# Kernel optimization log

Hardware: AMD Instinct MI355X
Metric: run time of the kernel (lower is better)

The kernel has to match this reference:

```python
import jax, jax.numpy as jnp
import numpy as np

B, C, H, W = 2, 256, 32, 32
PK, CK = 256, 256


def setup_inputs() -> dict:
    key = jax.random.key(0)
    ks = jax.random.split(key, 9)
    s = 1.0 / np.sqrt(C)
    return {
        'x': jax.random.normal(ks[0], (B, C, H, W), jnp.float32),
        'primary_indices': jax.random.randint(ks[1], (B, PK), 0, B * H * W),
        'compare_indices': jax.random.randint(ks[2], (B, CK), 0, B * H * W),
        'pre_w': jax.random.uniform(ks[3], (3, C, C), jnp.float32, -s, s),
        'pre_b': jax.random.uniform(ks[4], (3, C), jnp.float32, -s, s),
        'post_w': jax.random.uniform(ks[5], (2, C, C), jnp.float32, -s, s),
        'post_b': jax.random.uniform(ks[6], (2, C), jnp.float32, -s, s),
        'post_out_w': jax.random.uniform(ks[7], (2, C), jnp.float32, -s, s),
        'post_out_b': jax.random.uniform(ks[8], (2,), jnp.float32, -s, s),
    }


def reference(x, primary_indices, compare_indices, pre_w, pre_b,
              post_w, post_b, post_out_w, post_out_b):
    # pre_compare: stack of 1x1 convs (c->c->c->c), ReLU between layers
    h = x
    for i in range(3):
        h = jnp.einsum('bchw,oc->bohw', h, pre_w[i]) + pre_b[i][None, :, None, None]
        if i < 2:
            h = jax.nn.relu(h)
    bs, c, hh, ww = h.shape
    # flatten to [bs*h*w, c] node features (matches torch transpose+reshape)
    flat = h.reshape(bs, c, hh * ww).transpose(0, 2, 1).reshape(bs * hh * ww, c)
    # gather primary / compare node features with global flat indices
    xp = flat[primary_indices.reshape(-1)].reshape(bs, -1, c).transpose(0, 2, 1)  # [b,c,pk]
    xc = flat[compare_indices.reshape(-1)].reshape(bs, -1, c).transpose(0, 2, 1)  # [b,c,ck]
    # broadcast pairwise squared difference -> [b,c,pk,ck]
    xx = (xp[:, :, :, None] - xc[:, :, None, :]) ** 2
    # post_compare: 1x1 conv stack c->c->c->2, ReLU between layers
    g = xx
    for i in range(2):
        g = jax.nn.relu(jnp.einsum('bcpq,oc->bopq', g, post_w[i]) + post_b[i][None, :, None, None])
    out = jnp.einsum('bcpq,oc->bopq', g, post_out_w) + post_out_b[None, :, None, None]
    return out  # [b, 2, pk, ck]
```

## Files before the change

### kernel.cpp

```cpp
#include <hip/hip_runtime.h>

typedef unsigned short u16;
typedef short bf16x8 __attribute__((ext_vector_type(8)));
typedef float f32x4 __attribute__((ext_vector_type(4)));
typedef u16 u16x4 __attribute__((ext_vector_type(4)));

__device__ __forceinline__ float b2f(u16 h) {
  unsigned u = ((unsigned)h) << 16;
  return __builtin_bit_cast(float, u);
}
__device__ __forceinline__ u16 f2b(float f) {
  unsigned u = __builtin_bit_cast(unsigned, f);
  u = u + 0x7fffu + ((u >> 16) & 1u);
  return (u16)(u >> 16);
}
__device__ __forceinline__ void gld_lds16(const void* g, void* l) {
  __builtin_amdgcn_global_load_lds(
      (__attribute__((address_space(1))) void*)(g),
      (__attribute__((address_space(3))) void*)(l), 16, 0, 0);
}

__global__ void dense_edge_prep(const float* __restrict__ x,
                                const float* __restrict__ pre_w,
                                const float* __restrict__ post_w,
                                u16* __restrict__ wb, u16* __restrict__ xt) {
  const int blk = blockIdx.x;
  const int t = threadIdx.x;
  if (blk < 160) {
    const int id = blk * 256 + t;
    const int layer = id >> 13;
    const int sid = id & 8191;
    const int m = sid >> 5;
    const int s8 = sid & 31;
    const float* src = (layer < 2) ? (post_w + layer * 65536)
                                   : (pre_w + (layer - 2) * 65536);
    u16* dst = wb + layer * 65536;
    f32x4 a = *(const f32x4*)(src + m * 256 + s8 * 8);
    f32x4 c = *(const f32x4*)(src + m * 256 + s8 * 8 + 4);
    bf16x8 o;
#pragma unroll
    for (int j = 0; j < 4; j++) o[j] = (short)f2b(a[j]);
#pragma unroll
    for (int j = 0; j < 4; j++) o[4 + j] = (short)f2b(c[j]);
    *(bf16x8*)(dst + (s8 * 256 + m) * 8) = o;
  } else {
    __shared__ float tile[32 * 65];
    const int xb = blk - 160;
    const int b = xb >> 7;
    const int ct = (xb >> 4) & 7;
    const int ht = xb & 15;
    const int c0 = ct * 32, hw0 = ht * 64;
#pragma unroll
    for (int rep = 0; rep < 8; rep++) {
      const int idx = rep * 256 + t;
      const int cl = idx >> 6, hl = idx & 63;
      tile[cl * 65 + hl] = x[(b * 256 + c0 + cl) * 1024 + hw0 + hl];
    }
    __syncthreads();
    const int hl = t >> 2, c8 = t & 3;
    bf16x8 o;
#pragma unroll
    for (int i = 0; i < 8; i++) o[i] = (short)f2b(tile[(c8 * 8 + i) * 65 + hl]);
    *(bf16x8*)(xt + (b * 1024 + hw0 + hl) * 256 + c0 + c8 * 8) = o;
  }
}

__global__ __launch_bounds__(256, 2) void dense_edge_pre(
    const u16* __restrict__ xt, const u16* __restrict__ wpre,
    const float* __restrict__ preb, u16* __restrict__ flat) {
  __shared__ u16 feat[2][4096];
  const int t = threadIdx.x;
  const int wv = t >> 6, ln = t & 63;
  const int nb = blockIdx.x * 16;
  const int q4 = ln >> 4, r15 = ln & 15;

#pragma unroll
  for (int i = 0; i < 2; i++) {
    const int slot = wv * 128 + i * 64 + ln;
    const int s8 = slot >> 4, nl = slot & 15;
    gld_lds16(xt + (nb + nl) * 256 + s8 * 8, &feat[0][slot * 8]);
  }
  __syncthreads();

#pragma unroll
  for (int l = 0; l < 3; l++) {
    const u16* wl = wpre + l * 65536;
    f32x4 acc[4];
    f32x4 zero = {0.f, 0.f, 0.f, 0.f};
#pragma unroll
    for (int mt = 0; mt < 4; mt++) acc[mt] = zero;
#pragma unroll
    for (int s = 0; s < 8; s++) {
      bf16x8 bv = *(const bf16x8*)(&feat[l & 1][((s * 4 + q4) * 16 + r15) * 8]);
#pragma unroll
      for (int mt = 0; mt < 4; mt++) {
        bf16x8 av = *(const bf16x8*)(wl + ((s * 4 + q4) * 256 + wv * 64 + mt * 16 + r15) * 8);
        acc[mt] = __builtin_amdgcn_mfma_f32_16x16x32_bf16(av, bv, acc[mt], 0, 0, 0);
      }
    }
    if (l < 2) {
#pragma unroll
      for (int mt = 0; mt < 4; mt++) {
        const int o = wv * 64 + mt * 16 + q4 * 4;
        f32x4 bb = *(const f32x4*)(preb + l * 256 + o);
        u16x4 pk;
#pragma unroll
        for (int r = 0; r < 4; r++) {
          float v = fmaxf(acc[mt][r] + bb[r], 0.f);
          pk[r] = f2b(v);
        }
        *(u16x4*)(&feat[(l + 1) & 1][((o >> 3) * 16 + r15) * 8 + (o & 7)]) = pk;
      }
      __syncthreads();
    } else {
#pragma unroll
      for (int mt = 0; mt < 4; mt++) {
        const int o = wv * 64 + mt * 16 + q4 * 4;
        f32x4 bb = *(const f32x4*)(preb + 512 + o);
        u16x4 pk;
#pragma unroll
        for (int r = 0; r < 4; r++) pk[r] = f2b(acc[mt][r] + bb[r]);
        *(u16x4*)(flat + (nb + r15) * 256 + o) = pk;
      }
    }
  }
}

__global__ __launch_bounds__(512, 2) void dense_edge_main(
    const u16* __restrict__ flat, const int* __restrict__ pidx,
    const int* __restrict__ cidx, const u16* __restrict__ w1s,
    const u16* __restrict__ w2s, const float* __restrict__ b1,
    const float* __restrict__ b2, const float* __restrict__ w3,
    const float* __restrict__ b3, float* __restrict__ out) {
  __shared__ u16 xxbuf[16384];
  __shared__ u16 t1buf[16384];
  __shared__ float pbuf[4][2][64];

  const int t = threadIdx.x;
  const int wv = t >> 6;
  const int ln = t & 63;
  const int q4 = ln >> 4, r15 = ln & 15;
  const bool prod = wv < 4;
  const int cw = wv & 3;
  const int blk = blockIdx.x;
  const int tile0 = blk * 8;
  const int b = tile0 >> 10;
  const int pt = (tile0 >> 5) & 31;
  const int qt0 = tile0 & 31;
  const int p0 = pt * 8;

  const u16* wsrc = prod ? w1s : w2s;
  bf16x8 af_w[4][8];
#pragma unroll
  for (int s = 0; s < 8; s++)
#pragma unroll
    for (int mt = 0; mt < 4; mt++)
      af_w[mt][s] = *(const bf16x8*)(wsrc + ((s * 4 + q4) * 256 + cw * 64 + mt * 16 + r15) * 8);

  int pn = 0;
  if (prod) pn = pidx[b * 256 + p0 + (ln >> 3)];
  const u16* prow = flat + pn * 256 + cw * 64;

#pragma unroll 1
  for (int j = 0; j <= 8; j++) {
    if (prod) {
      if (j < 8) {
        const int qn = cidx[b * 256 + (qt0 + j) * 8 + (ln & 7)];
        const u16* qrow = flat + qn * 256 + cw * 64;
#pragma unroll
        for (int i = 0; i < 8; i++) {
          bf16x8 av = *(const bf16x8*)(prow + i * 8);
          bf16x8 bv = *(const bf16x8*)(qrow + i * 8);
          bf16x8 ov;
#pragma unroll
          for (int jj = 0; jj < 8; jj++) {
            float d = b2f((u16)av[jj]) - b2f((u16)bv[jj]);
            ov[jj] = (short)f2b(d * d);
          }
          *(bf16x8*)(xxbuf + ((cw * 8 + i) * 64 + ln) * 8) = ov;
        }
      }
    } else if (j > 0) {
      f32x4 acc[4][4];
      {
        f32x4 zero = {0.f, 0.f, 0.f, 0.f};
#pragma unroll
        for (int mt = 0; mt < 4; mt++)
#pragma unroll
          for (int nt = 0; nt < 4; nt++) acc[mt][nt] = zero;
      }
#pragma unroll
      for (int s = 0; s < 8; s++) {
        bf16x8 bfr[4];
#pragma unroll
        for (int nt = 0; nt < 4; nt++)
          bfr[nt] = *(const bf16x8*)(t1buf + ((s * 4 + q4) * 64 + nt * 16 + r15) * 8);
#pragma unroll
        for (int mt = 0; mt < 4; mt++)
#pragma unroll
          for (int nt = 0; nt < 4; nt++)
            acc[mt][nt] = __builtin_amdgcn_mfma_f32_16x16x32_bf16(af_w[mt][s], bfr[nt], acc[mt][nt], 0, 0, 0);
      }
      float part[2][4] = {{0.f, 0.f, 0.f, 0.f}, {0.f, 0.f, 0.f, 0.f}};
#pragma unroll
      for (int mt = 0; mt < 4; mt++) {
        const int o = cw * 64 + mt * 16 + q4 * 4;
        f32x4 bb = *(const f32x4*)(b2 + o);
        f32x4 w3a = *(const f32x4*)(w3 + o);
        f32x4 w3b = *(const f32x4*)(w3 + 256 + o);
#pragma unroll
        for (int nt = 0; nt < 4; nt++) {
#pragma unroll
          for (int r = 0; r < 4; r++) {
            float v = fmaxf(acc[mt][nt][r] + bb[r], 0.f);
            part[0][nt] += v * w3a[r];
            part[1][nt] += v * w3b[r];
          }
        }
      }
#pragma unroll
      for (int o3 = 0; o3 < 2; o3++)
#pragma unroll
        for (int nt = 0; nt < 4; nt++) {
          part[o3][nt] += __shfl_xor(part[o3][nt], 16, 64);
          part[o3][nt] += __shfl_xor(part[o3][nt], 32, 64);
        }
      if (q4 == 0) {
#pragma unroll
        for (int o3 = 0; o3 < 2; o3++)
#pragma unroll
          for (int nt = 0; nt < 4; nt++)
            pbuf[cw][o3][nt * 16 + r15] = part[o3][nt];
      }
    }
    __syncthreads();

    if (prod) {
      if (j < 8) {
        f32x4 acc[4][4];
        {
          f32x4 zero = {0.f, 0.f, 0.f, 0.f};
#pragma unroll
          for (int mt = 0; mt < 4; mt++)
#pragma unroll
            for (int nt = 0; nt < 4; nt++) acc[mt][nt] = zero;
        }
#pragma unroll
        for (int s = 0; s < 8; s++) {
          bf16x8 bfr[4];
#pragma unroll
          for (int nt = 0; nt < 4; nt++)
            bfr[nt] = *(const bf16x8*)(xxbuf + ((s * 4 + q4) * 64 + nt * 16 + r15) * 8);
#pragma unroll
          for (int mt = 0; mt < 4; mt++)
#pragma unroll
            for (int nt = 0; nt < 4; nt++)
              acc[mt][nt] = __builtin_amdgcn_mfma_f32_16x16x32_bf16(af_w[mt][s], bfr[nt], acc[mt][nt], 0, 0, 0);
        }
#pragma unroll
        for (int mt = 0; mt < 4; mt++) {
          const int o = cw * 64 + mt * 16 + q4 * 4;
          f32x4 bb = *(const f32x4*)(b1 + o);
#pragma unroll
          for (int nt = 0; nt < 4; nt++) {
            const int nn = nt * 16 + r15;
            u16x4 pk;
#pragma unroll
            for (int r = 0; r < 4; r++) {
              float v = fmaxf(acc[mt][nt][r] + bb[r], 0.f);
              pk[r] = f2b(v);
            }
            *(u16x4*)(t1buf + ((o >> 3) * 64 + nn) * 8 + (o & 7)) = pk;
          }
        }
      }
    } else if (j > 0) {
      const int idx = t & 255;
      if (idx < 128) {
        const int o3 = idx >> 6;
        const int n = idx & 63;
        float v = pbuf[0][o3][n] + pbuf[1][o3][n] + pbuf[2][o3][n] + pbuf[3][o3][n] + b3[o3];
        out[((b * 2 + o3) * 256 + p0 + (n >> 3)) * 256 + (qt0 + j - 1) * 8 + (n & 7)] = v;
      }
    }
    __syncthreads();
  }
}

extern "C" void kernel_launch(void* const* d_in, const int* in_sizes, int n_in,
                              void* d_out, int out_size, void* d_ws, size_t ws_size,
                              hipStream_t stream) {
  (void)in_sizes; (void)n_in; (void)out_size; (void)ws_size;
  const float* x          = (const float*)d_in[0];
  const int*   pidx       = (const int*)d_in[1];
  const int*   cidx       = (const int*)d_in[2];
  const float* pre_w      = (const float*)d_in[3];
  const float* pre_b      = (const float*)d_in[4];
  const float* post_w     = (const float*)d_in[5];
  const float* post_b     = (const float*)d_in[6];
  const float* post_out_w = (const float*)d_in[7];
  const float* post_out_b = (const float*)d_in[8];
  float* out = (float*)d_out;

  u16* ws   = (u16*)d_ws;
  u16* wb   = ws;
  u16* w1s  = wb;
  u16* w2s  = wb + 65536;
  u16* wpre = wb + 131072;
  u16* xt   = ws + 327680;
  u16* flat = ws + 851968;

  dense_edge_prep<<<416, 256, 0, stream>>>(x, pre_w, post_w, wb, xt);
  dense_edge_pre<<<128, 256, 0, stream>>>(xt, wpre, pre_b, flat);
  dense_edge_main<<<256, 512, 0, stream>>>(flat, pidx, cidx, w1s, w2s,
                                           post_b, post_b + 256,
                                           post_out_w, post_out_b, out);
}
```

Before: 124.3 us.

## Pipeline main kernel with double-buffered t1 and async compare-row prefetch

Restructures the main loop so each iteration has a single phase between barriers. Producer waves run GEMM1 into a double-buffered t1buf while consumer waves run GEMM2 on the previous tile, and the final output write is deferred by one iteration. Compare rows are now prefetched into swizzled LDS with async global-to-LDS loads one tile ahead. The squared-difference work is spread across all 8 waves, with primary rows held in registers. bf16 conversion switches to a packed convert builtin when available. Costs are more LDS use, which may lower occupancy, and a somewhat trickier schedule.

```diff
diff --git a/kernel.cpp b/kernel.cpp
--- a/kernel.cpp
+++ b/kernel.cpp
@@ -13,6 +13,37 @@
   unsigned u = __builtin_bit_cast(unsigned, f);
   u = u + 0x7fffu + ((u >> 16) & 1u);
   return (u16)(u >> 16);
+}
+
+#if defined(__has_builtin)
+#if __has_builtin(__builtin_amdgcn_cvt_pk_bf16_f32)
+#define HAVE_CVT_PK_BF16 1
+#endif
+#endif
+
+__device__ __forceinline__ unsigned f2b_pk(float a, float b) {
+#ifdef HAVE_CVT_PK_BF16
+  auto v = __builtin_amdgcn_cvt_pk_bf16_f32(a, b);
+  unsigned r;
+  __builtin_memcpy(&r, &v, 4);
+  return r;
+#else
+  return (unsigned)f2b(a) | (((unsigned)f2b(b)) << 16);
+#endif
+}
+__device__ __forceinline__ bf16x8 pack8(const float* v) {
+  union { unsigned u[4]; bf16x8 o; } r;
+  r.u[0] = f2b_pk(v[0], v[1]);
+  r.u[1] = f2b_pk(v[2], v[3]);
+  r.u[2] = f2b_pk(v[4], v[5]);
+  r.u[3] = f2b_pk(v[6], v[7]);
+  return r.o;
+}
+__device__ __forceinline__ u16x4 pack4(float a, float b, float c, float d) {
+  union { unsigned u[2]; u16x4 o; } r;
+  r.u[0] = f2b_pk(a, b);
+  r.u[1] = f2b_pk(c, d);
+  return r.o;
 }
 __device__ __forceinline__ void gld_lds16(const void* g, void* l) {
   __builtin_amdgcn_global_load_lds(
@@ -37,12 +68,8 @@
     u16* dst = wb + layer * 65536;
     f32x4 a = *(const f32x4*)(src + m * 256 + s8 * 8);
     f32x4 c = *(const f32x4*)(src + m * 256 + s8 * 8 + 4);
-    bf16x8 o;
-#pragma unroll
-    for (int j = 0; j < 4; j++) o[j] = (short)f2b(a[j]);
-#pragma unroll
-    for (int j = 0; j < 4; j++) o[4 + j] = (short)f2b(c[j]);
-    *(bf16x8*)(dst + (s8 * 256 + m) * 8) = o;
+    float tmp[8] = {a[0], a[1], a[2], a[3], c[0], c[1], c[2], c[3]};
+    *(bf16x8*)(dst + (s8 * 256 + m) * 8) = pack8(tmp);
   } else {
     __shared__ float tile[32 * 65];
     const int xb = blk - 160;
@@ -58,10 +85,10 @@
     }
     __syncthreads();
     const int hl = t >> 2, c8 = t & 3;
-    bf16x8 o;
-#pragma unroll
-    for (int i = 0; i < 8; i++) o[i] = (short)f2b(tile[(c8 * 8 + i) * 65 + hl]);
-    *(bf16x8*)(xt + (b * 1024 + hw0 + hl) * 256 + c0 + c8 * 8) = o;
+    float tmp[8];
+#pragma unroll
+    for (int i = 0; i < 8; i++) tmp[i] = tile[(c8 * 8 + i) * 65 + hl];
+    *(bf16x8*)(xt + (b * 1024 + hw0 + hl) * 256 + c0 + c8 * 8) = pack8(tmp);
   }
 }
 
@@ -103,13 +130,9 @@
       for (int mt = 0; mt < 4; mt++) {
         const int o = wv * 64 + mt * 16 + q4 * 4;
         f32x4 bb = *(const f32x4*)(preb + l * 256 + o);
-        u16x4 pk;
-#pragma unroll
-        for (int r = 0; r < 4; r++) {
-          float v = fmaxf(acc[mt][r] + bb[r], 0.f);
-          pk[r] = f2b(v);
-        }
-        *(u16x4*)(&feat[(l + 1) & 1][((o >> 3) * 16 + r15) * 8 + (o & 7)]) = pk;
+        *(u16x4*)(&feat[(l + 1) & 1][((o >> 3) * 16 + r15) * 8 + (o & 7)]) =
+            pack4(fmaxf(acc[mt][0] + bb[0], 0.f), fmaxf(acc[mt][1] + bb[1], 0.f),
+                  fmaxf(acc[mt][2] + bb[2], 0.f), fmaxf(acc[mt][3] + bb[3], 0.f));
       }
       __syncthreads();
     } else {
@@ -117,10 +140,9 @@
       for (int mt = 0; mt < 4; mt++) {
         const int o = wv * 64 + mt * 16 + q4 * 4;
         f32x4 bb = *(const f32x4*)(preb + 512 + o);
-        u16x4 pk;
-#pragma unroll
-        for (int r = 0; r < 4; r++) pk[r] = f2b(acc[mt][r] + bb[r]);
-        *(u16x4*)(flat + (nb + r15) * 256 + o) = pk;
+        *(u16x4*)(flat + (nb + r15) * 256 + o) =
+            pack4(acc[mt][0] + bb[0], acc[mt][1] + bb[1],
+                  acc[mt][2] + bb[2], acc[mt][3] + bb[3]);
       }
     }
   }
@@ -133,7 +155,8 @@
     const float* __restrict__ b2, const float* __restrict__ w3,
     const float* __restrict__ b3, float* __restrict__ out) {
   __shared__ u16 xxbuf[16384];
-  __shared__ u16 t1buf[16384];
+  __shared__ u16 t1buf[2][16384];
+  __shared__ u16 qrows[2][2048];
   __shared__ float pbuf[4][2][64];
 
   const int t = threadIdx.x;
@@ -157,44 +180,110 @@
     for (int mt = 0; mt < 4; mt++)
       af_w[mt][s] = *(const bf16x8*)(wsrc + ((s * 4 + q4) * 256 + cw * 64 + mt * 16 + r15) * 8);
 
-  int pn = 0;
-  if (prod) pn = pidx[b * 256 + p0 + (ln >> 3)];
-  const u16* prow = flat + pn * 256 + cw * 64;
+  const int pn = pidx[b * 256 + p0 + (ln >> 3)];
+  bf16x8 pch[4];
+#pragma unroll
+  for (int i = 0; i < 4; i++)
+    pch[i] = *(const bf16x8*)(flat + pn * 256 + wv * 32 + i * 8);
+
+  if (prod) {
+    const int row = 2 * cw + (ln >> 5);
+    const int qn = cidx[b * 256 + qt0 * 8 + row];
+    const int m = ln & 31;
+    gld_lds16(flat + qn * 256 + ((m ^ (row & 7)) * 8),
+              (u16*)qrows[0] + cw * 512 + ln * 8);
+  }
+  __syncthreads();
 
 #pragma unroll 1
   for (int j = 0; j <= 8; j++) {
+    if (j < 8) {
+      if (prod && j + 1 < 8) {
+        const int row = 2 * cw + (ln >> 5);
+        const int qn = cidx[b * 256 + (qt0 + j + 1) * 8 + row];
+        const int m = ln & 31;
+        gld_lds16(flat + qn * 256 + ((m ^ (row & 7)) * 8),
+                  (u16*)qrows[(j + 1) & 1] + cw * 512 + ln * 8);
+      }
+      {
+        const int q = ln & 7;
+        const u16* qbase = qrows[j & 1] + q * 256;
+#pragma unroll
+        for (int i = 0; i < 4; i++) {
+          const int c = wv * 4 + i;
+          bf16x8 qv = *(const bf16x8*)(qbase + ((c ^ q) * 8));
+          bf16x8 pv = pch[i];
+          float d[8];
+#pragma unroll
+          for (int jj = 0; jj < 8; jj++) {
+            float dv = b2f((u16)pv[jj]) - b2f((u16)qv[jj]);
+            d[jj] = dv * dv;
+          }
+          *(bf16x8*)(xxbuf + (c * 64 + ln) * 8) = pack8(d);
+        }
+      }
+    }
+    if (!prod && j >= 2) {
+      const int idx = cw * 64 + ln;
+      if (idx < 128) {
+        const int o3 = idx >> 6;
+        const int n = idx & 63;
+        float v = b3[o3] + pbuf[0][o3][n] + pbuf[1][o3][n] + pbuf[2][o3][n] + pbuf[3][o3][n];
+        out[((b * 2 + o3) * 256 + p0 + (n >> 3)) * 256 + (qt0 + j - 2) * 8 + (n & 7)] = v;
+      }
+    }
+    __syncthreads();
+
     if (prod) {
       if (j < 8) {
-        const int qn = cidx[b * 256 + (qt0 + j) * 8 + (ln & 7)];
-        const u16* qrow = flat + qn * 256 + cw * 64;
-#pragma unroll
-        for (int i = 0; i < 8; i++) {
-          bf16x8 av = *(const bf16x8*)(prow + i * 8);
-          bf16x8 bv = *(const bf16x8*)(qrow + i * 8);
-          bf16x8 ov;
-#pragma unroll
-          for (int jj = 0; jj < 8; jj++) {
-            float d = b2f((u16)av[jj]) - b2f((u16)bv[jj]);
-            ov[jj] = (short)f2b(d * d);
+        f32x4 acc[4][4];
+        f32x4 zero = {0.f, 0.f, 0.f, 0.f};
+#pragma unroll
+        for (int mt = 0; mt < 4; mt++)
+#pragma unroll
+          for (int nt = 0; nt < 4; nt++) acc[mt][nt] = zero;
+#pragma unroll
+        for (int s = 0; s < 8; s++) {
+          bf16x8 bfr[4];
+#pragma unroll
+          for (int nt = 0; nt < 4; nt++)
+            bfr[nt] = *(const bf16x8*)(xxbuf + ((s * 4 + q4) * 64 + nt * 16 + r15) * 8);
+#pragma unroll
+          for (int mt = 0; mt < 4; mt++)
+#pragma unroll
+            for (int nt = 0; nt < 4; nt++)
+              acc[mt][nt] = __builtin_amdgcn_mfma_f32_16x16x32_bf16(af_w[mt][s], bfr[nt], acc[mt][nt], 0, 0, 0);
+        }
+        u16* tdst = t1buf[j & 1];
+#pragma unroll
+        for (int mt = 0; mt < 4; mt++) {
+          const int o = cw * 64 + mt * 16 + q4 * 4;
+          f32x4 bb = *(const f32x4*)(b1 + o);
+#pragma unroll
+          for (int nt = 0; nt < 4; nt++) {
+            const int nn = nt * 16 + r15;
+            *(u16x4*)(tdst + ((o >> 3) * 64 + nn) * 8 + (o & 7)) =
+                pack4(fmaxf(acc[mt][nt][0] + bb[0], 0.f),
+                      fmaxf(acc[mt][nt][1] + bb[1], 0.f),
+                      fmaxf(acc[mt][nt][2] + bb[2], 0.f),
+                      fmaxf(acc[mt][nt][3] + bb[3], 0.f));
           }
-          *(bf16x8*)(xxbuf + ((cw * 8 + i) * 64 + ln) * 8) = ov;
-        }
-      }
-    } else if (j > 0) {
+        }
+      }
+    } else if (j >= 1) {
+      const u16* tsrc = t1buf[(j - 1) & 1];
       f32x4 acc[4][4];
-      {
-        f32x4 zero = {0.f, 0.f, 0.f, 0.f};
-#pragma unroll
-        for (int mt = 0; mt < 4; mt++)
-#pragma unroll
-          for (int nt = 0; nt < 4; nt++) acc[mt][nt] = zero;
-      }
+      f32x4 zero = {0.f, 0.f, 0.f, 0.f};
+#pragma unroll
+      for (int mt = 0; mt < 4; mt++)
+#pragma unroll
+        for (int nt = 0; nt < 4; nt++) acc[mt][nt] = zero;
 #pragma unroll
       for (int s = 0; s < 8; s++) {
         bf16x8 bfr[4];
 #pragma unroll
         for (int nt = 0; nt < 4; nt++)
-          bfr[nt] = *(const bf16x8*)(t1buf + ((s * 4 + q4) * 64 + nt * 16 + r15) * 8);
+          bfr[nt] = *(const bf16x8*)(tsrc + ((s * 4 + q4) * 64 + nt * 16 + r15) * 8);
 #pragma unroll
         for (int mt = 0; mt < 4; mt++)
 #pragma unroll
@@ -234,56 +323,16 @@
       }
     }
     __syncthreads();
-
-    if (prod) {
-      if (j < 8) {
-        f32x4 acc[4][4];
-        {
-          f32x4 zero = {0.f, 0.f, 0.f, 0.f};
-#pragma unroll
-          for (int mt = 0; mt < 4; mt++)
-#pragma unroll
-            for (int nt = 0; nt < 4; nt++) acc[mt][nt] = zero;
-        }
-#pragma unroll
-        for (int s = 0; s < 8; s++) {
-          bf16x8 bfr[4];
-#pragma unroll
-          for (int nt = 0; nt < 4; nt++)
-            bfr[nt] = *(const bf16x8*)(xxbuf + ((s * 4 + q4) * 64 + nt * 16 + r15) * 8);
-#pragma unroll
-          for (int mt = 0; mt < 4; mt++)
-#pragma unroll
-            for (int nt = 0; nt < 4; nt++)
-              acc[mt][nt] = __builtin_amdgcn_mfma_f32_16x16x32_bf16(af_w[mt][s], bfr[nt], acc[mt][nt], 0, 0, 0);
-        }
-#pragma unroll
-        for (int mt = 0; mt < 4; mt++) {
-          const int o = cw * 64 + mt * 16 + q4 * 4;
-          f32x4 bb = *(const f32x4*)(b1 + o);
-#pragma unroll
-          for (int nt = 0; nt < 4; nt++) {
-            const int nn = nt * 16 + r15;
-            u16x4 pk;
-#pragma unroll
-            for (int r = 0; r < 4; r++) {
-              float v = fmaxf(acc[mt][nt][r] + bb[r], 0.f);
-              pk[r] = f2b(v);
-            }
-            *(u16x4*)(t1buf + ((o >> 3) * 64 + nn) * 8 + (o & 7)) = pk;
-          }
-        }
-      }
-    } else if (j > 0) {
-      const int idx = t & 255;
-      if (idx < 128) {
-        const int o3 = idx >> 6;
-        const int n = idx & 63;
-        float v = pbuf[0][o3][n] + pbuf[1][o3][n] + pbuf[2][o3][n] + pbuf[3][o3][n] + b3[o3];
-        out[((b * 2 + o3) * 256 + p0 + (n >> 3)) * 256 + (qt0 + j - 1) * 8 + (n & 7)] = v;
-      }
-    }
-    __syncthreads();
+  }
+
+  if (!prod) {
+    const int idx = cw * 64 + ln;
+    if (idx < 128) {
+      const int o3 = idx >> 6;
+      const int n = idx & 63;
+      float v = b3[o3] + pbuf[0][o3][n] + pbuf[1][o3][n] + pbuf[2][o3][n] + pbuf[3][o3][n];
+      out[((b * 2 + o3) * 256 + p0 + (n >> 3)) * 256 + (qt0 + 7) * 8 + (n & 7)] = v;
+    }
   }
 }
 
@@ -303,14 +352,13 @@
   float* out = (float*)d_out;
 
   u16* ws   = (u16*)d_ws;
-  u16* wb   = ws;
-  u16* w1s  = wb;
-  u16* w2s  = wb + 65536;
-  u16* wpre = wb + 131072;
+  u16* w1s  = ws;
+  u16* w2s  = ws + 65536;
+  u16* wpre = ws + 131072;
   u16* xt   = ws + 327680;
   u16* flat = ws + 851968;
 
-  dense_edge_prep<<<416, 256, 0, stream>>>(x, pre_w, post_w, wb, xt);
+  dense_edge_prep<<<416, 256, 0, stream>>>(x, pre_w, post_w, ws, xt);
   dense_edge_pre<<<128, 256, 0, stream>>>(xt, wpre, pre_b, flat);
   dense_edge_main<<<256, 512, 0, stream>>>(flat, pidx, cidx, w1s, w2s,
                                            post_b, post_b + 256,
```

After: 144.8 us. +16.5%, slower.
